# Kernel optimization log

Hardware: AMD Instinct MI355X
Metric: run time of the kernel (lower is better)

Reference implementation:

```python
import jax, jax.numpy as jnp
import numpy as np

B, H, W = 16, 180, 240  # dim=(180,240), batch inferred from last event in torch code
N = 8_000_000


def setup_inputs() -> dict:
    key = jax.random.key(0)
    k0, k1, k2, k3, k4 = jax.random.split(key, 5)
    x = jax.random.randint(k0, (N,), 0, W).astype(jnp.float32)
    y = jax.random.randint(k1, (N,), 0, H).astype(jnp.float32)
    t = jax.random.uniform(k2, (N,), dtype=jnp.float32)
    p = (jax.random.randint(k3, (N,), 0, 2) * 2 - 1).astype(jnp.float32)  # polarity in {-1,1}
    # b sorted so events[-1,-1] == B-1, matching how torch code infers B
    b = jnp.sort(jax.random.randint(k4, (N,), 0, B)).astype(jnp.float32)
    events = jnp.stack([x, y, t, p, b], axis=1)  # [N,5]
    return {"events": events}


def reference(events):
    x, y, t, p, b = (events[:, i] for i in range(5))
    bi = b.astype(jnp.int32)

    # per-batch time normalization: t /= max(t within batch)
    tmax = jax.ops.segment_max(t, bi, num_segments=B)
    t = t / tmax[bi]
    p = (p + 1.0) / 2.0  # computed (as in torch) but unused downstream

    # full-res event-count histogram: idx = x + W*y + W*H*b
    idx_c = (x + W * y + W * H * b).astype(jnp.int32)
    container = jnp.zeros(B * H * W, jnp.int32).at[idx_c].add(1, mode="drop")
    container = container.reshape(B, H, W)

    # half-res counter/timer; replicate torch float floordiv exactly:
    # idx = x//2 + (W*y)//4 + (W*H*b)//4
    idx_k = (jnp.floor_divide(x, 2.0)
             + jnp.floor_divide(W * y, 4.0)
             + jnp.floor_divide(W * H * b, 4.0)).astype(jnp.int32)
    nvox = B * (H // 2) * (W // 2)
    counter = jnp.zeros(nvox, jnp.int32).at[idx_k].add(1, mode="drop").astype(jnp.float32)
    timer = jnp.zeros(nvox, jnp.float32).at[idx_k].add(t, mode="drop")
    timer = timer / jnp.where(counter == 0, 1.0, counter)  # mean timestamp per voxel
    counter = counter.reshape(B, H // 2, W // 2)
    timer = timer.reshape(B, H // 2, W // 2)

    # strided diffs on the full-res histogram
    dy = container[:, ::2] - container[:, 1::2]          # [B, H/2, W]
    diff_y = dy[:, :, ::2] + dy[:, :, 1::2]              # [B, H/2, W/2]
    dx = container[:, :, ::2] - container[:, :, 1::2]    # [B, H, W/2]
    diff_x = dx[:, 1::2] + dx[:, ::2]                    # [B, H/2, W/2]

    return container, counter, timer, diff_x, diff_y
```

## Files before the change

kernel.cpp:

```cpp
#include <hip/hip_runtime.h>
#include <stdint.h>

constexpr int NB    = 16;
constexpr int NH    = 180;
constexpr int NW    = 240;
constexpr int FULL  = NB * NH * NW;
constexpr int SEG   = (NH / 2) * (NW / 2);
constexpr int HALF  = NB * SEG;
constexpr int CELLS = NH * NW;
constexpr int H4W   = CELLS / 8;
constexpr int EVT   = 1024;
constexpr int NBPB  = 16;
constexpr int NBLK  = NB * NBPB;
constexpr int RT    = 43;
constexpr int TSX   = SEG + 60;

constexpr int O_TMAXB = 0;
constexpr int O_BLDP  = NBLK;
constexpr int O_PRIV  = O_BLDP + NBLK * 60;
constexpr int FB_TMAX  = 0;
constexpr int FB_BLEED = 16;
constexpr int FB_CONT  = FB_BLEED + HALF;
constexpr int FB_TSUM  = FB_CONT + FULL;
constexpr int FB_CNT   = FB_TSUM + HALF;
constexpr int ZFALL    = FB_CNT + HALF;

__global__ __launch_bounds__(EVT) void k_merged(const float* __restrict__ ev, int n,
                                                unsigned int* __restrict__ ws,
                                                unsigned int* __restrict__ h4p,
                                                float* __restrict__ tsp) {
    float* tmax_blk = (float*)(ws + O_TMAXB);
    float* bleed_p  = (float*)(ws + O_BLDP);

    __shared__ unsigned int h4[H4W];
    __shared__ float        ts[TSX];
    __shared__ int          sbe[2];
    __shared__ unsigned int bsm;
    int tid = threadIdx.x;
    int b0 = blockIdx.x / NBPB;
    int r  = blockIdx.x - b0 * NBPB;

    if (tid < 2) {
        int target = b0 + tid;
        int lo = 0, hi = n;
        while (lo < hi) {
            int mid = (lo + hi) >> 1;
            float v = ev[(size_t)5 * mid + 4];
            if (v < (float)target) lo = mid + 1; else hi = mid;
        }
        sbe[tid] = lo;
    } else {
        uint4 z = {0u, 0u, 0u, 0u};
        uint4* h4v = (uint4*)h4;
        uint4* tsv = (uint4*)ts;
        int t2 = tid - 2;
        for (int i = t2; i < H4W / 4; i += EVT - 2) h4v[i] = z;
        for (int i = t2; i < SEG / 4; i += EVT - 2) tsv[i] = z;
        if (t2 < TSX - SEG) ts[SEG + t2] = 0.0f;
        if (tid == 2) bsm = 0u;
    }
    __syncthreads();

    int sb = sbe[0], eb = sbe[1];
    long long len = (long long)(eb - sb);
    int s = sb + (int)(len * r / NBPB);
    int e = sb + (int)(len * (r + 1) / NBPB);

    float tloc = 0.0f;

    auto proc = [&](float fx, float fy, float t) {
        int xi = (int)fx, yi = (int)fy;
        int cell = xi + NW * yi;
        int loc  = (xi >> 1) + (NW / 4) * yi;
        tloc = fmaxf(tloc, t);
        atomicAdd(&h4[cell >> 3], 1u << ((cell & 7) * 4));
        atomicAdd(&ts[loc], t);
    };

    if (s < e) {
        int as_ = min((s + 3) & ~3, e);
        for (int i = s + tid; i < as_; i += EVT) {
            const float* rr = ev + (size_t)5 * i;
            proc(rr[0], rr[1], rr[2]);
        }
        int ng = (e - as_) >> 2;
        const float4* e4 = (const float4*)ev;
        size_t qbase = (size_t)5 * (size_t)(as_ >> 2);
        for (int g = tid; g < ng; g += 2 * EVT) {
            int g2 = g + EVT;
            size_t qb = qbase + (size_t)5 * g;
            float4 q0 = e4[qb], q1 = e4[qb + 1], q2 = e4[qb + 2],
                   q3 = e4[qb + 3], q4 = e4[qb + 4];
            if (g2 < ng) {
                size_t qc = qbase + (size_t)5 * g2;
                float4 p0 = e4[qc], p1 = e4[qc + 1], p2 = e4[qc + 2],
                       p3 = e4[qc + 3], p4 = e4[qc + 4];
                proc(q0.x, q0.y, q0.z);
                proc(q1.y, q1.z, q1.w);
                proc(q2.z, q2.w, q3.x);
                proc(q3.w, q4.x, q4.y);
                proc(p0.x, p0.y, p0.z);
                proc(p1.y, p1.z, p1.w);
                proc(p2.z, p2.w, p3.x);
                proc(p3.w, p4.x, p4.y);
            } else {
                proc(q0.x, q0.y, q0.z);
                proc(q1.y, q1.z, q1.w);
                proc(q2.z, q2.w, q3.x);
                proc(q3.w, q4.x, q4.y);
            }
        }
        for (int i = as_ + (ng << 2) + tid; i < e; i += EVT) {
            const float* rr = ev + (size_t)5 * i;
            proc(rr[0], rr[1], rr[2]);
        }
    }

#pragma unroll
    for (int o = 32; o > 0; o >>= 1) tloc = fmaxf(tloc, __shfl_xor(tloc, o));
    if ((tid & 63) == 0) atomicMax(&bsm, __float_as_uint(tloc));
    __syncthreads();

    {
        const uint4* h4v = (const uint4*)h4;
        const uint4* tsv = (const uint4*)ts;
        uint4* dh = (uint4*)(h4p + (size_t)blockIdx.x * H4W);
        uint4* dt = (uint4*)(tsp + (size_t)blockIdx.x * SEG);
        for (int i = tid; i < H4W / 4; i += EVT) dh[i] = h4v[i];
        for (int i = tid; i < SEG / 4; i += EVT) dt[i] = tsv[i];
    }
    if (tid < 60) bleed_p[blockIdx.x * 60 + tid] = ts[SEG + tid];
    if (tid == 0) tmax_blk[blockIdx.x] = __uint_as_float(bsm);
}

__global__ __launch_bounds__(256) void k_reduce(const unsigned int* __restrict__ ws,
                                                const unsigned int* __restrict__ h4p,
                                                const float* __restrict__ tsp,
                                                float* __restrict__ out) {
    const float* tmax_blk = (const float*)(ws + O_TMAXB);
    const float* bleed_p  = (const float*)(ws + O_BLDP);

    __shared__ float stm[2];
    int tid  = threadIdx.x;
    int b    = blockIdx.x / RT;
    int tile = blockIdx.x - b * RT;

    if (tid < 32) {
        int which = tid >> 4;
        int k = tid & 15;
        int bb = b - which;
        float v = (bb >= 0) ? tmax_blk[bb * NBPB + k] : 0.0f;
#pragma unroll
        for (int o = 8; o > 0; o >>= 1) v = fmaxf(v, __shfl_xor(v, o));
        if (k == 0) stm[which] = v;
    }
    __syncthreads();

    int rem = tile * 256 + tid;
    if (rem >= SEG) return;
    int v = b * SEG + rem;
    int i = rem / (NW / 2);
    int j = rem - i * (NW / 2);
    int cbl = 480 * i + 2 * j;
    int cbg = CELLS * b + cbl;

    unsigned c00 = 0, c01 = 0, c10 = 0, c11 = 0, oc = 0;
    float tsum = 0.0f, bl = 0.0f;

    bool prev = false;
    int ocell;
    if (j >= 60)      ocell = cbl + 120;
    else if (i >= 1)  ocell = cbl - 120;
    else { prev = true; ocell = 43080 + 2 * j; }

    int w0i = cbl >> 3, nib = (cbl & 7) * 4;
    int w1i = w0i + 30;
    int owi = ocell >> 3, onib = (ocell & 7) * 4;

    int base = b * NBPB;
#pragma unroll
    for (int k = 0; k < NBPB; ++k) {
        const unsigned int* hp = h4p + (size_t)(base + k) * H4W;
        unsigned w0 = hp[w0i], w1 = hp[w1i], wo = hp[owi];
        float tv = tsp[(size_t)(base + k) * SEG + rem];
        c00 += (w0 >> nib) & 15u;  c01 += (w0 >> (nib + 4)) & 15u;
        c10 += (w1 >> nib) & 15u;  c11 += (w1 >> (nib + 4)) & 15u;
        oc  += ((wo >> onib) & 15u) + ((wo >> (onib + 4)) & 15u);
        tsum += tv;
    }
    if (prev) {
        oc = 0;
        if (b >= 1) {
            int pb = (b - 1) * NBPB;
#pragma unroll
            for (int k = 0; k < NBPB; ++k) {
                unsigned wo = h4p[(size_t)(pb + k) * H4W + owi];
                oc += ((wo >> onib) & 15u) + ((wo >> (onib + 4)) & 15u);
                bl += bleed_p[(pb + k) * 60 + j];
            }
        }
    }
    unsigned cnt = c00 + c01 + oc;

    out[cbg]          = (float)c00;
    out[cbg + 1]      = (float)c01;
    out[cbg + NW]     = (float)c10;
    out[cbg + NW + 1] = (float)c11;
    out[FULL + v] = (float)cnt;

    float tm = stm[0];
    if (!(tm > 0.0f)) tm = 1.0f;
    float tmp = stm[1];
    if (!(tmp > 0.0f)) tmp = 1.0f;
    float s = tsum / tm + bl / tmp;
    out[FULL + HALF + v] = s / (float)(cnt == 0 ? 1u : cnt);

    out[FULL + 2 * HALF + v] = (float)((int)c00 - (int)c01 + (int)c10 - (int)c11);
    out[FULL + 3 * HALF + v] = (float)((int)c00 + (int)c01 - (int)c10 - (int)c11);
}


__global__ __launch_bounds__(256) void f_init(unsigned int* __restrict__ ws, int bound) {
    int i = blockIdx.x * 256 + threadIdx.x;
    int stride = gridDim.x * 256;
    for (; i < bound; i += stride) ws[i] = 0u;
}

__global__ __launch_bounds__(256) void f_events(const float* __restrict__ ev, int n,
                                                unsigned int* __restrict__ ws) {
    unsigned int* tmaxb = ws + FB_TMAX;
    int*   cont  = (int*)(ws + FB_CONT);
    int*   cnt   = (int*)(ws + FB_CNT);
    float* tsum  = (float*)(ws + FB_TSUM);
    float* bleed = (float*)(ws + FB_BLEED);
    __shared__ unsigned int smax[NB];
    if (threadIdx.x < NB) smax[threadIdx.x] = 0u;
    __syncthreads();
    int chunk = (n + gridDim.x - 1) / (int)gridDim.x;
    int start = blockIdx.x * chunk;
    int end   = min(start + chunk, n);
    for (int i = start + (int)threadIdx.x; i < end; i += (int)blockDim.x) {
        const float* r = ev + (size_t)5 * (size_t)i;
        int xi = (int)r[0], yi = (int)r[1], bi = (int)r[4];
        float t = r[2];
        atomicMax(&smax[bi], __float_as_uint(t));
        atomicAdd(&cont[xi + NW * yi + CELLS * bi], 1);
        int loc = (xi >> 1) + (NW / 4) * yi;
        int ik  = loc + SEG * bi;
        if (ik < HALF) {
            atomicAdd(&cnt[ik], 1);
            if (loc >= SEG) atomicAdd(&bleed[ik], t);
            else            atomicAdd(&tsum[ik], t);
        }
    }
    __syncthreads();
    if (threadIdx.x < NB) {
        unsigned v = smax[threadIdx.x];
        if (v) atomicMax(&tmaxb[threadIdx.x], v);
    }
}

__global__ __launch_bounds__(256) void f_epilogue(const unsigned int* __restrict__ ws,
                                                  float* __restrict__ out) {
    const unsigned int* tmaxb = ws + FB_TMAX;
    const int*   cont  = (const int*)(ws + FB_CONT);
    const int*   cnt   = (const int*)(ws + FB_CNT);
    const float* tsum  = (const float*)(ws + FB_TSUM);
    const float* bleed = (const float*)(ws + FB_BLEED);
    int v = blockIdx.x * blockDim.x + threadIdx.x;
    if (v >= HALF) return;
    int b   = v / SEG;
    int rem = v - b * SEG;
    int i   = rem / (NW / 2);
    int j   = rem - i * (NW / 2);
    int cbase = b * CELLS + 480 * i + 2 * j;
    int c00 = cont[cbase],      c01 = cont[cbase + 1];
    int c10 = cont[cbase + NW], c11 = cont[cbase + NW + 1];
    out[cbase]          = (float)c00;
    out[cbase + 1]      = (float)c01;
    out[cbase + NW]     = (float)c10;
    out[cbase + NW + 1] = (float)c11;
    int c = cnt[v];
    out[FULL + v] = (float)c;
    float tm  = __uint_as_float(tmaxb[b]);
    if (!(tm > 0.0f)) tm = 1.0f;
    float tmp = (b > 0) ? __uint_as_float(tmaxb[b - 1]) : 1.0f;
    if (!(tmp > 0.0f)) tmp = 1.0f;
    float s   = tsum[v] / tm + bleed[v] / tmp;
    out[FULL + HALF + v] = s / (float)(c == 0 ? 1 : c);
    out[FULL + 2 * HALF + v] = (float)(c00 - c01 + c10 - c11);
    out[FULL + 3 * HALF + v] = (float)(c00 + c01 - c10 - c11);
}

extern "C" void kernel_launch(void* const* d_in, const int* in_sizes, int n_in,
                              void* d_out, int out_size, void* d_ws, size_t ws_size,
                              hipStream_t stream) {
    const float* ev = (const float*)d_in[0];
    int n = in_sizes[0] / 5;
    unsigned int* ws = (unsigned int*)d_ws;
    float* out = (float*)d_out;

    size_t need = (size_t)(O_PRIV + NBLK * (H4W + SEG)) * 4u;

    if (ws_size >= need && n > 0) {
        unsigned int* h4p = ws + O_PRIV;
        float*        tsp = (float*)(ws + O_PRIV + NBLK * H4W);
        hipLaunchKernelGGL(k_merged, dim3(NBLK), dim3(EVT), 0, stream, ev, n, ws, h4p, tsp);
        hipLaunchKernelGGL(k_reduce, dim3(NB * RT), dim3(256), 0, stream, ws, h4p, tsp, out);
    } else {
        hipLaunchKernelGGL(f_init, dim3(512), dim3(256), 0, stream, ws, ZFALL);
        hipLaunchKernelGGL(f_events, dim3(2048), dim3(256), 0, stream, ev, n, ws);
        hipLaunchKernelGGL(f_epilogue, dim3((HALF + 255) / 256), dim3(256), 0, stream, ws, out);
    }
}
```

Measured before the change: 244.5 us.

## Store per-block timestamp partials as packed bf16 and unroll event loads 4x

The per-block partial timestamp sums written to the workspace are now rounded to bf16 and packed two per word, which halves the partial-sum traffic between the histogram kernel and the reduce kernel. The event loop also issues four groups of float4 loads per iteration instead of two, so more memory requests are in flight. The bf16 rounding loses precision in the timer output, and the larger unroll raises register pressure in 1024-thread blocks.

```diff
diff --git a/kernel.cpp b/kernel.cpp
--- a/kernel.cpp
+++ b/kernel.cpp
@@ -14,6 +14,7 @@
 constexpr int NBLK  = NB * NBPB;
 constexpr int RT    = 43;
 constexpr int TSX   = SEG + 60;
+constexpr int TSW   = SEG / 2;
 
 constexpr int O_TMAXB = 0;
 constexpr int O_BLDP  = NBLK;
@@ -25,10 +26,15 @@
 constexpr int FB_CNT   = FB_TSUM + HALF;
 constexpr int ZFALL    = FB_CNT + HALF;
 
+__device__ __forceinline__ unsigned bf16rne(float f) {
+    unsigned u = __float_as_uint(f);
+    return (u + 0x7fffu + ((u >> 16) & 1u)) >> 16;
+}
+
 __global__ __launch_bounds__(EVT) void k_merged(const float* __restrict__ ev, int n,
                                                 unsigned int* __restrict__ ws,
                                                 unsigned int* __restrict__ h4p,
-                                                float* __restrict__ tsp) {
+                                                unsigned int* __restrict__ tsb) {
     float* tmax_blk = (float*)(ws + O_TMAXB);
     float* bleed_p  = (float*)(ws + O_BLDP);
 
@@ -86,29 +92,31 @@
         int ng = (e - as_) >> 2;
         const float4* e4 = (const float4*)ev;
         size_t qbase = (size_t)5 * (size_t)(as_ >> 2);
-        for (int g = tid; g < ng; g += 2 * EVT) {
-            int g2 = g + EVT;
+        int g = tid;
+        for (; g + 3 * EVT < ng; g += 4 * EVT) {
+            float4 q[4][5];
+#pragma unroll
+            for (int u = 0; u < 4; ++u) {
+                size_t qb = qbase + (size_t)5 * (g + u * EVT);
+#pragma unroll
+                for (int w = 0; w < 5; ++w) q[u][w] = e4[qb + w];
+            }
+#pragma unroll
+            for (int u = 0; u < 4; ++u) {
+                proc(q[u][0].x, q[u][0].y, q[u][0].z);
+                proc(q[u][1].y, q[u][1].z, q[u][1].w);
+                proc(q[u][2].z, q[u][2].w, q[u][3].x);
+                proc(q[u][3].w, q[u][4].x, q[u][4].y);
+            }
+        }
+        for (; g < ng; g += EVT) {
             size_t qb = qbase + (size_t)5 * g;
             float4 q0 = e4[qb], q1 = e4[qb + 1], q2 = e4[qb + 2],
                    q3 = e4[qb + 3], q4 = e4[qb + 4];
-            if (g2 < ng) {
-                size_t qc = qbase + (size_t)5 * g2;
-                float4 p0 = e4[qc], p1 = e4[qc + 1], p2 = e4[qc + 2],
-                       p3 = e4[qc + 3], p4 = e4[qc + 4];
-                proc(q0.x, q0.y, q0.z);
-                proc(q1.y, q1.z, q1.w);
-                proc(q2.z, q2.w, q3.x);
-                proc(q3.w, q4.x, q4.y);
-                proc(p0.x, p0.y, p0.z);
-                proc(p1.y, p1.z, p1.w);
-                proc(p2.z, p2.w, p3.x);
-                proc(p3.w, p4.x, p4.y);
-            } else {
-                proc(q0.x, q0.y, q0.z);
-                proc(q1.y, q1.z, q1.w);
-                proc(q2.z, q2.w, q3.x);
-                proc(q3.w, q4.x, q4.y);
-            }
+            proc(q0.x, q0.y, q0.z);
+            proc(q1.y, q1.z, q1.w);
+            proc(q2.z, q2.w, q3.x);
+            proc(q3.w, q4.x, q4.y);
         }
         for (int i = as_ + (ng << 2) + tid; i < e; i += EVT) {
             const float* rr = ev + (size_t)5 * i;
@@ -123,11 +131,11 @@
 
     {
         const uint4* h4v = (const uint4*)h4;
-        const uint4* tsv = (const uint4*)ts;
         uint4* dh = (uint4*)(h4p + (size_t)blockIdx.x * H4W);
-        uint4* dt = (uint4*)(tsp + (size_t)blockIdx.x * SEG);
         for (int i = tid; i < H4W / 4; i += EVT) dh[i] = h4v[i];
-        for (int i = tid; i < SEG / 4; i += EVT) dt[i] = tsv[i];
+        unsigned int* dt = tsb + (size_t)blockIdx.x * TSW;
+        for (int i = tid; i < TSW; i += EVT)
+            dt[i] = bf16rne(ts[2 * i]) | (bf16rne(ts[2 * i + 1]) << 16);
     }
     if (tid < 60) bleed_p[blockIdx.x * 60 + tid] = ts[SEG + tid];
     if (tid == 0) tmax_blk[blockIdx.x] = __uint_as_float(bsm);
@@ -135,7 +143,7 @@
 
 __global__ __launch_bounds__(256) void k_reduce(const unsigned int* __restrict__ ws,
                                                 const unsigned int* __restrict__ h4p,
-                                                const float* __restrict__ tsp,
+                                                const unsigned int* __restrict__ tsb,
                                                 float* __restrict__ out) {
     const float* tmax_blk = (const float*)(ws + O_TMAXB);
     const float* bleed_p  = (const float*)(ws + O_BLDP);
@@ -176,17 +184,18 @@
     int w0i = cbl >> 3, nib = (cbl & 7) * 4;
     int w1i = w0i + 30;
     int owi = ocell >> 3, onib = (ocell & 7) * 4;
+    int twi = rem >> 1, tsh = (rem & 1) * 16;
 
     int base = b * NBPB;
 #pragma unroll
     for (int k = 0; k < NBPB; ++k) {
         const unsigned int* hp = h4p + (size_t)(base + k) * H4W;
         unsigned w0 = hp[w0i], w1 = hp[w1i], wo = hp[owi];
-        float tv = tsp[(size_t)(base + k) * SEG + rem];
+        unsigned tw = tsb[(size_t)(base + k) * TSW + twi];
         c00 += (w0 >> nib) & 15u;  c01 += (w0 >> (nib + 4)) & 15u;
         c10 += (w1 >> nib) & 15u;  c11 += (w1 >> (nib + 4)) & 15u;
         oc  += ((wo >> onib) & 15u) + ((wo >> (onib + 4)) & 15u);
-        tsum += tv;
+        tsum += __uint_as_float(((tw >> tsh) & 0xffffu) << 16);
     }
     if (prev) {
         oc = 0;
@@ -300,13 +309,13 @@
     unsigned int* ws = (unsigned int*)d_ws;
     float* out = (float*)d_out;
 
-    size_t need = (size_t)(O_PRIV + NBLK * (H4W + SEG)) * 4u;
+    size_t need = (size_t)(O_PRIV + NBLK * (H4W + TSW)) * 4u;
 
     if (ws_size >= need && n > 0) {
         unsigned int* h4p = ws + O_PRIV;
-        float*        tsp = (float*)(ws + O_PRIV + NBLK * H4W);
-        hipLaunchKernelGGL(k_merged, dim3(NBLK), dim3(EVT), 0, stream, ev, n, ws, h4p, tsp);
-        hipLaunchKernelGGL(k_reduce, dim3(NB * RT), dim3(256), 0, stream, ws, h4p, tsp, out);
+        unsigned int* tsb = ws + O_PRIV + NBLK * H4W;
+        hipLaunchKernelGGL(k_merged, dim3(NBLK), dim3(EVT), 0, stream, ev, n, ws, h4p, tsb);
+        hipLaunchKernelGGL(k_reduce, dim3(NB * RT), dim3(256), 0, stream, ws, h4p, tsb, out);
     } else {
         hipLaunchKernelGGL(f_init, dim3(512), dim3(256), 0, stream, ws, ZFALL);
         hipLaunchKernelGGL(f_events, dim3(2048), dim3(256), 0, stream, ev, n, ws);
```

Result: no change. 245.4 us (+0.3%).
